# Kernel optimization log

Hardware: AMD Instinct MI355X
Metric: run time of the kernel (lower is better)

The kernel has to match this reference:

```python
import math
import jax, jax.numpy as jnp
import numpy as np

B, N = 8, 2048
IN_DIM = COND_DIM = ATTN_DIM = OUT_DIM = 128
NUM_HEADS = 4
DH = ATTN_DIM // NUM_HEADS  # 32


def setup_inputs() -> dict:
    key = jax.random.key(0)
    ks = jax.random.split(key, 10)
    s_in = 1.0 / math.sqrt(IN_DIM)
    s_cd = 1.0 / math.sqrt(COND_DIM)
    return {
        "x": jax.random.normal(ks[0], (B, N, IN_DIM), jnp.float32),
        "cond": jax.random.normal(ks[1], (B, N, COND_DIM), jnp.float32),
        "flags": jnp.ones((B, N, 1), jnp.float32),
        "attention_mask": jax.random.normal(ks[2], (B, N, N), jnp.float32),
        # Linear params (stored [in, out]; torch Linear is x @ W.T + b)
        "Wq": jax.random.uniform(ks[3], (IN_DIM, ATTN_DIM), jnp.float32, -s_in, s_in),
        "bq": jax.random.uniform(ks[4], (ATTN_DIM,), jnp.float32, -s_in, s_in),
        "Wk": jax.random.uniform(ks[5], (COND_DIM, ATTN_DIM), jnp.float32, -s_cd, s_cd),
        "bk": jax.random.uniform(ks[6], (ATTN_DIM,), jnp.float32, -s_cd, s_cd),
        "Wv": jax.random.uniform(ks[7], (COND_DIM, OUT_DIM), jnp.float32, -s_cd, s_cd),
        "bv": jax.random.uniform(ks[8], (OUT_DIM,), jnp.float32, -s_cd, s_cd),
    }


def reference(x, cond, flags, attention_mask, Wq, bq, Wk, bk, Wv, bv):
    # flags is accepted but unused, matching the original forward.
    b, n, _ = x.shape
    Q = (x @ Wq + bq).reshape(b, n, NUM_HEADS, DH)     # channel-split heads
    K = (cond @ Wk + bk).reshape(b, n, NUM_HEADS, DH)
    V = cond @ Wv + bv                                 # [B, N, OUT_DIM]
    # per-head scores, scaled by sqrt(out_dim) as in the original
    S = jnp.einsum("bnhd,bmhd->hbnm", Q, K) / math.sqrt(OUT_DIM)
    A = jnp.tanh(attention_mask[None] + S)             # tanh activation, not softmax
    A = A.mean(axis=0)                                 # head-mean -> [B, N, N]
    return jnp.einsum("bnm,bmd->bnd", A, V)
```

## Files before the change

### kernel.cpp

```cpp
#include <hip/hip_runtime.h>
#include <hip/hip_bf16.h>

typedef __attribute__((ext_vector_type(4))) float f32x4;
typedef __attribute__((ext_vector_type(8))) short bf16x8;

#define MFMA16(A, B, C) __builtin_amdgcn_mfma_f32_16x16x32_bf16(A, B, C, 0, 0, 0)

#define C2 2.8853900817779268f
#define QS (2.8853900817779268f / 11.313708498984761f)

__device__ __forceinline__ unsigned cvtpk_bf16(float lo, float hi) {
    unsigned r;
    asm("v_cvt_pk_bf16_f32 %0, %1, %2" : "=v"(r) : "v"(lo), "v"(hi));
    return r;
}

__device__ __forceinline__ bf16x8 pack8(float4 a, float4 b) {
    union { unsigned u[4]; bf16x8 v; } u;
    u.u[0] = cvtpk_bf16(a.x, a.y);
    u.u[1] = cvtpk_bf16(a.z, a.w);
    u.u[2] = cvtpk_bf16(b.x, b.y);
    u.u[3] = cvtpk_bf16(b.z, b.w);
    return u.v;
}

__device__ __forceinline__ void gload_lds16(const void* g, void* l) {
    __builtin_amdgcn_global_load_lds(
        (const __attribute__((address_space(1))) unsigned int*)g,
        (__attribute__((address_space(3))) unsigned int*)l, 16, 0, 0);
}

__global__ void prep_weights(const float* __restrict__ Wq, const float* __restrict__ bq,
                             const float* __restrict__ Wk, const float* __restrict__ bk,
                             const float* __restrict__ Wv, const float* __restrict__ bv,
                             __hip_bfloat16* __restrict__ Wqt, __hip_bfloat16* __restrict__ Wkt,
                             __hip_bfloat16* __restrict__ Wvt, float* __restrict__ bias) {
    int i = blockIdx.x * 256 + threadIdx.x;
    int k = i >> 7, o = i & 127;
    Wqt[o * 128 + k] = __float2bfloat16(Wq[i] * QS);
    Wkt[o * 128 + k] = __float2bfloat16(Wk[i]);
    Wvt[o * 128 + k] = __float2bfloat16(Wv[i] * 0.25f);
    if (i < 128) {
        bias[i]       = bq[i] * QS;
        bias[128 + i] = bk[i];
        bias[256 + i] = bv[i] * 0.25f;
    }
}

__global__ __launch_bounds__(256) void proj_qkv(
        const float* __restrict__ x, const float* __restrict__ cond,
        const __hip_bfloat16* __restrict__ Wqt, const __hip_bfloat16* __restrict__ Wkt,
        const __hip_bfloat16* __restrict__ Wvt, const float* __restrict__ bias,
        __hip_bfloat16* __restrict__ Qo, __hip_bfloat16* __restrict__ Ko,
        __hip_bfloat16* __restrict__ Vt) {
    const int lane = threadIdx.x & 63, wv = threadIdx.x >> 6;
    const int l15 = lane & 15, g = lane >> 4;
    const int row0 = blockIdx.x * 64 + wv * 16;

    f32x4 qa[8], ka[8], va[8];
#pragma unroll
    for (int ot = 0; ot < 8; ++ot) {
        float b0 = bias[16 * ot + l15];
        float b1 = bias[128 + 16 * ot + l15];
        float b2 = bias[256 + 16 * ot + l15];
        qa[ot] = (f32x4){b0, b0, b0, b0};
        ka[ot] = (f32x4){b1, b1, b1, b1};
        va[ot] = (f32x4){b2, b2, b2, b2};
    }

    const float* xp = x    + (size_t)(row0 + l15) * 128 + 8 * g;
    const float* cp = cond + (size_t)(row0 + l15) * 128 + 8 * g;
#pragma unroll
    for (int kk = 0; kk < 4; ++kk) {
        float4 x0 = *(const float4*)(xp + 32 * kk);
        float4 x1 = *(const float4*)(xp + 32 * kk + 4);
        float4 c0 = *(const float4*)(cp + 32 * kk);
        float4 c1 = *(const float4*)(cp + 32 * kk + 4);
        bf16x8 xa = pack8(x0, x1);
        bf16x8 ca = pack8(c0, c1);
#pragma unroll
        for (int ot = 0; ot < 8; ++ot) {
            const int wo = (16 * ot + l15) * 128 + 32 * kk + 8 * g;
            qa[ot] = MFMA16(xa, *(const bf16x8*)(Wqt + wo), qa[ot]);
            ka[ot] = MFMA16(ca, *(const bf16x8*)(Wkt + wo), ka[ot]);
            va[ot] = MFMA16(ca, *(const bf16x8*)(Wvt + wo), va[ot]);
        }
    }

#pragma unroll
    for (int ot = 0; ot < 8; ++ot)
#pragma unroll
        for (int r = 0; r < 4; ++r) {
            size_t idx = (size_t)(row0 + 4 * g + r) * 128 + 16 * ot + l15;
            Qo[idx] = __float2bfloat16(qa[ot][r]);
            Ko[idx] = __float2bfloat16(ka[ot][r]);
        }
    const int bb = row0 >> 11, nn = (row0 & 2047) + 4 * g;
#pragma unroll
    for (int ot = 0; ot < 8; ++ot) {
        uint2 pr;
        pr.x = cvtpk_bf16(va[ot][0], va[ot][1]);
        pr.y = cvtpk_bf16(va[ot][2], va[ot][3]);
        *(uint2*)((unsigned short*)Vt + ((size_t)bb * 128 + 16 * ot + l15) * 2048 + nn) = pr;
    }
}

__global__ __launch_bounds__(512) void attn_main(
        const __hip_bfloat16* __restrict__ Q, const __hip_bfloat16* __restrict__ K,
        const __hip_bfloat16* __restrict__ Vt, const float* __restrict__ mask,
        float* __restrict__ out) {
    __shared__ __align__(16) char Kl[2][16384];
    __shared__ __align__(16) char Vl[2][16384];
    __shared__ __align__(16) char Al[64 * 144];

    const int lane = threadIdx.x & 63, w = threadIdx.x >> 6;
    const int l15 = lane & 15, g = lane >> 4;
    const int qw = w & 3, mw = w >> 2, dw = mw;
    const int qt = blockIdx.x & 31;
    const int mh = (blockIdx.x >> 5) & 1;
    const int b  = blockIdx.x >> 6;
    const int n0 = qt * 64;
    const int mh0 = mh * 1024;

    const __hip_bfloat16* Qb = Q + ((size_t)b * 2048 + n0 + qw * 16) * 128;
    const char* Kg = (const char*)(K + (size_t)b * 2048 * 128);
    const char* Vg = (const char*)(Vt + (size_t)b * 128 * 2048);
    const float* mrow = mask + ((size_t)b * 2048 + n0 + qw * 16 + l15) * 2048
                        + mh0 + mw * 32 + 4 * g;

    bf16x8 qf[4];
#pragma unroll
    for (int h = 0; h < 4; ++h)
        qf[h] = *(const bf16x8*)(Qb + l15 * 128 + 32 * h + 8 * g);

    f32x4 oacc[4];
#pragma unroll
    for (int dtl = 0; dtl < 4; ++dtl) oacc[dtl] = (f32x4){0.f, 0.f, 0.f, 0.f};
    const f32x4 zero = (f32x4){0.f, 0.f, 0.f, 0.f};

    auto STAGE = [&](int m0g, int bi) {
#pragma unroll
        for (int i = 0; i < 2; ++i) {
            const int t = w * 2 + i;
            const int o = t * 1024 + lane * 16;
            const int kr = o >> 8, kc = o & 255;
            gload_lds16(Kg + (size_t)(m0g + kr) * 256 + (kc ^ ((kr & 7) << 4)),
                        &Kl[bi][t * 1024]);
            const int vr = o >> 7, vc = o & 127;
            gload_lds16(Vg + (size_t)vr * 4096 + (size_t)m0g * 2 + (vc ^ ((vr & 7) << 4)),
                        &Vl[bi][t * 1024]);
        }
    };

    STAGE(mh0, 0);
    f32x4 mkc0 = *(const f32x4*)(mrow);
    f32x4 mkc1 = *(const f32x4*)(mrow + 16);
    asm volatile("s_waitcnt vmcnt(0)" ::: "memory");
    __builtin_amdgcn_s_barrier();

#pragma unroll 2
    for (int c = 0; c < 16; ++c) {
        const int bi = c & 1;
        const int m0g = mh0 + c * 64;
        if (c < 15) STAGE(m0g + 64, bi ^ 1);
        f32x4 mkn0, mkn1;
        if (c < 15) {
            mkn0 = *(const f32x4*)(mrow + (c + 1) * 64);
            mkn1 = *(const f32x4*)(mrow + (c + 1) * 64 + 16);
        }

#pragma unroll
        for (int st = 0; st < 2; ++st) {
            const int mr = mw * 32 + st * 16 + l15;
            const char* kb = &Kl[bi][mr * 256];
            const int sw = (mr & 7) << 4;
            f32x4 s0 = MFMA16(*(const bf16x8*)(kb + ((g * 16) ^ sw)),       qf[0], zero);
            f32x4 s1 = MFMA16(*(const bf16x8*)(kb + ((64 + g * 16) ^ sw)),  qf[1], zero);
            f32x4 s2 = MFMA16(*(const bf16x8*)(kb + ((128 + g * 16) ^ sw)), qf[2], zero);
            f32x4 s3 = MFMA16(*(const bf16x8*)(kb + ((192 + g * 16) ^ sw)), qf[3], zero);
            const f32x4 mk = st ? mkc1 : mkc0;
            float acd[4];
#pragma unroll
            for (int r = 0; r < 4; ++r) {
                float m2 = mk[r] * C2;
                float e0 = __builtin_amdgcn_exp2f(m2 + s0[r]);
                float e1 = __builtin_amdgcn_exp2f(m2 + s1[r]);
                float e2 = __builtin_amdgcn_exp2f(m2 + s2[r]);
                float e3 = __builtin_amdgcn_exp2f(m2 + s3[r]);
                float rs = __builtin_amdgcn_rcpf(1.f + e0) + __builtin_amdgcn_rcpf(1.f + e1)
                         + __builtin_amdgcn_rcpf(1.f + e2) + __builtin_amdgcn_rcpf(1.f + e3);
                acd[r] = 4.f - 2.f * rs;
            }
            uint2 pk;
            pk.x = cvtpk_bf16(acd[0], acd[1]);
            pk.y = cvtpk_bf16(acd[2], acd[3]);
            *(uint2*)(Al + (qw * 16 + l15) * 144 + (mw * 32 + st * 16 + 4 * g) * 2) = pk;
        }

        asm volatile("s_waitcnt lgkmcnt(0)" ::: "memory");
        __builtin_amdgcn_s_barrier();

#pragma unroll
        for (int ks = 0; ks < 2; ++ks) {
            bf16x8 af = *(const bf16x8*)(Al + (qw * 16 + l15) * 144 + (ks * 32 + 8 * g) * 2);
#pragma unroll
            for (int dtl = 0; dtl < 4; ++dtl) {
                const int dr = dw * 64 + dtl * 16 + l15;
                bf16x8 vf = *(const bf16x8*)(
                    &Vl[bi][dr * 128 + ((ks * 64 + g * 16) ^ ((dr & 7) << 4))]);
                oacc[dtl] = MFMA16(af, vf, oacc[dtl]);
            }
        }

        asm volatile("s_waitcnt vmcnt(0)" ::: "memory");
        __builtin_amdgcn_s_barrier();

        mkc0 = mkn0;
        mkc1 = mkn1;
    }

    float* ob = out + ((size_t)b * 2048 + n0 + qw * 16) * 128 + dw * 64;
#pragma unroll
    for (int dtl = 0; dtl < 4; ++dtl)
#pragma unroll
        for (int r = 0; r < 4; ++r)
            unsafeAtomicAdd(&ob[(size_t)(4 * g + r) * 128 + dtl * 16 + l15], oacc[dtl][r]);
}

extern "C" void kernel_launch(void* const* d_in, const int* in_sizes, int n_in,
                              void* d_out, int out_size, void* d_ws, size_t ws_size,
                              hipStream_t stream) {
    const float* x    = (const float*)d_in[0];
    const float* cond = (const float*)d_in[1];
    const float* mask = (const float*)d_in[3];
    const float* Wq = (const float*)d_in[4];
    const float* bq = (const float*)d_in[5];
    const float* Wk = (const float*)d_in[6];
    const float* bk = (const float*)d_in[7];
    const float* Wv = (const float*)d_in[8];
    const float* bv = (const float*)d_in[9];
    float* out = (float*)d_out;

    char* ws = (char*)d_ws;
    __hip_bfloat16* Qo  = (__hip_bfloat16*)(ws);
    __hip_bfloat16* Ko  = (__hip_bfloat16*)(ws + (4  << 20));
    __hip_bfloat16* Vt  = (__hip_bfloat16*)(ws + (8  << 20));
    __hip_bfloat16* Wqt = (__hip_bfloat16*)(ws + (12 << 20));
    __hip_bfloat16* Wkt = (__hip_bfloat16*)(ws + (12 << 20) + 32768);
    __hip_bfloat16* Wvt = (__hip_bfloat16*)(ws + (12 << 20) + 65536);
    float*          bias = (float*)(ws + (12 << 20) + 98304);

    hipMemsetAsync(d_out, 0, (size_t)out_size * sizeof(float), stream);

    prep_weights<<<64, 256, 0, stream>>>(Wq, bq, Wk, bk, Wv, bv, Wqt, Wkt, Wvt, bias);
    proj_qkv<<<256, 256, 0, stream>>>(x, cond, Wqt, Wkt, Wvt, bias, Qo, Ko, Vt);
    attn_main<<<512, 512, 0, stream>>>(Qo, Ko, Vt, mask, out);
}
```

Baseline: 88.02 us.

## Skew PV matmul one chunk behind scores, read V directly from global

Stops staging V tiles in LDS and has each wave load its V fragments straight from global memory. It double-buffers the attention-weight tile so the PV MFMA for chunk c-1 runs after the score phase of chunk c. This removes one barrier per iteration and an epilogue handles the final chunk. The K swizzle widens from 8 to 16 rows to cut LDS bank conflicts. The cost is uncoalesced per-lane global V reads that rely on cache, and the loop waits on vmcnt(0) for those loads at every barrier.

```diff
diff --git a/kernel.cpp b/kernel.cpp
--- a/kernel.cpp
+++ b/kernel.cpp
@@ -110,8 +110,7 @@
         const __hip_bfloat16* __restrict__ Vt, const float* __restrict__ mask,
         float* __restrict__ out) {
     __shared__ __align__(16) char Kl[2][16384];
-    __shared__ __align__(16) char Vl[2][16384];
-    __shared__ __align__(16) char Al[64 * 144];
+    __shared__ __align__(16) char Al[2][64 * 144];
 
     const int lane = threadIdx.x & 63, w = threadIdx.x >> 6;
     const int l15 = lane & 15, g = lane >> 4;
@@ -124,7 +123,7 @@
 
     const __hip_bfloat16* Qb = Q + ((size_t)b * 2048 + n0 + qw * 16) * 128;
     const char* Kg = (const char*)(K + (size_t)b * 2048 * 128);
-    const char* Vg = (const char*)(Vt + (size_t)b * 128 * 2048);
+    const unsigned short* Vg = (const unsigned short*)Vt + (size_t)b * 128 * 2048;
     const float* mrow = mask + ((size_t)b * 2048 + n0 + qw * 16 + l15) * 2048
                         + mh0 + mw * 32 + 4 * g;
 
@@ -138,21 +137,18 @@
     for (int dtl = 0; dtl < 4; ++dtl) oacc[dtl] = (f32x4){0.f, 0.f, 0.f, 0.f};
     const f32x4 zero = (f32x4){0.f, 0.f, 0.f, 0.f};
 
-    auto STAGE = [&](int m0g, int bi) {
+    auto STAGE_K = [&](int m0g, int bi) {
 #pragma unroll
         for (int i = 0; i < 2; ++i) {
             const int t = w * 2 + i;
             const int o = t * 1024 + lane * 16;
             const int kr = o >> 8, kc = o & 255;
-            gload_lds16(Kg + (size_t)(m0g + kr) * 256 + (kc ^ ((kr & 7) << 4)),
+            gload_lds16(Kg + (size_t)(m0g + kr) * 256 + (kc ^ ((kr & 15) << 4)),
                         &Kl[bi][t * 1024]);
-            const int vr = o >> 7, vc = o & 127;
-            gload_lds16(Vg + (size_t)vr * 4096 + (size_t)m0g * 2 + (vc ^ ((vr & 7) << 4)),
-                        &Vl[bi][t * 1024]);
         }
     };
 
-    STAGE(mh0, 0);
+    STAGE_K(mh0, 0);
     f32x4 mkc0 = *(const f32x4*)(mrow);
     f32x4 mkc1 = *(const f32x4*)(mrow + 16);
     asm volatile("s_waitcnt vmcnt(0)" ::: "memory");
@@ -161,10 +157,9 @@
 #pragma unroll 2
     for (int c = 0; c < 16; ++c) {
         const int bi = c & 1;
-        const int m0g = mh0 + c * 64;
-        if (c < 15) STAGE(m0g + 64, bi ^ 1);
         f32x4 mkn0, mkn1;
         if (c < 15) {
+            STAGE_K(mh0 + (c + 1) * 64, bi ^ 1);
             mkn0 = *(const f32x4*)(mrow + (c + 1) * 64);
             mkn1 = *(const f32x4*)(mrow + (c + 1) * 64 + 16);
         }
@@ -173,7 +168,7 @@
         for (int st = 0; st < 2; ++st) {
             const int mr = mw * 32 + st * 16 + l15;
             const char* kb = &Kl[bi][mr * 256];
-            const int sw = (mr & 7) << 4;
+            const int sw = (mr & 15) << 4;
             f32x4 s0 = MFMA16(*(const bf16x8*)(kb + ((g * 16) ^ sw)),       qf[0], zero);
             f32x4 s1 = MFMA16(*(const bf16x8*)(kb + ((64 + g * 16) ^ sw)),  qf[1], zero);
             f32x4 s2 = MFMA16(*(const bf16x8*)(kb + ((128 + g * 16) ^ sw)), qf[2], zero);
@@ -194,29 +189,43 @@
             uint2 pk;
             pk.x = cvtpk_bf16(acd[0], acd[1]);
             pk.y = cvtpk_bf16(acd[2], acd[3]);
-            *(uint2*)(Al + (qw * 16 + l15) * 144 + (mw * 32 + st * 16 + 4 * g) * 2) = pk;
-        }
-
-        asm volatile("s_waitcnt lgkmcnt(0)" ::: "memory");
+            *(uint2*)(&Al[bi][(qw * 16 + l15) * 144 + (mw * 32 + st * 16 + 4 * g) * 2]) = pk;
+        }
+
+        if (c > 0) {
+            const int m0p = mh0 + (c - 1) * 64;
+#pragma unroll
+            for (int ks = 0; ks < 2; ++ks) {
+                bf16x8 af = *(const bf16x8*)(
+                    &Al[bi ^ 1][(qw * 16 + l15) * 144 + (ks * 32 + 8 * g) * 2]);
+#pragma unroll
+                for (int dtl = 0; dtl < 4; ++dtl) {
+                    const int dr = dw * 64 + dtl * 16 + l15;
+                    bf16x8 vf = *(const bf16x8*)(Vg + (size_t)dr * 2048 + m0p + ks * 32 + 8 * g);
+                    oacc[dtl] = MFMA16(af, vf, oacc[dtl]);
+                }
+            }
+        }
+
+        asm volatile("s_waitcnt vmcnt(0) lgkmcnt(0)" ::: "memory");
         __builtin_amdgcn_s_barrier();
-
+        mkc0 = mkn0;
+        mkc1 = mkn1;
+    }
+
+    {
+        const int m0p = mh0 + 15 * 64;
 #pragma unroll
         for (int ks = 0; ks < 2; ++ks) {
-            bf16x8 af = *(const bf16x8*)(Al + (qw * 16 + l15) * 144 + (ks * 32 + 8 * g) * 2);
+            bf16x8 af = *(const bf16x8*)(
+                &Al[1][(qw * 16 + l15) * 144 + (ks * 32 + 8 * g) * 2]);
 #pragma unroll
             for (int dtl = 0; dtl < 4; ++dtl) {
                 const int dr = dw * 64 + dtl * 16 + l15;
-                bf16x8 vf = *(const bf16x8*)(
-                    &Vl[bi][dr * 128 + ((ks * 64 + g * 16) ^ ((dr & 7) << 4))]);
+                bf16x8 vf = *(const bf16x8*)(Vg + (size_t)dr * 2048 + m0p + ks * 32 + 8 * g);
                 oacc[dtl] = MFMA16(af, vf, oacc[dtl]);
             }
         }
-
-        asm volatile("s_waitcnt vmcnt(0)" ::: "memory");
-        __builtin_amdgcn_s_barrier();
-
-        mkc0 = mkn0;
-        mkc1 = mkn1;
     }
 
     float* ob = out + ((size_t)b * 2048 + n0 + qw * 16) * 128 + dw * 64;
```

After: 123.3 us. 40.1% more time.
